# Kernel optimization log

Measured on AMD Instinct MI355X. Metric: run time of the kernel, lower is better.

Reference implementation:

```python
import jax, jax.numpy as jnp
import numpy as np

N = 12288      # num nodes == in_num_dim (num_center_nodes)
D_IN = 512     # in_node_dim
D_EMB = 128    # embed_dim
D_OUT = 64     # out_dim
E = 393216     # num edges (avg degree 32)
NEG_SLOPE = 0.2  # GATConv default negative_slope


def _glorot(k, shape):
    lim = float(np.sqrt(6.0 / (shape[0] + shape[1])))
    return jax.random.uniform(k, shape, jnp.float32, -lim, lim)


def setup_inputs() -> dict:
    key = jax.random.key(0)
    ks = jax.random.split(key, 13)
    x = jax.random.normal(ks[0], (N, D_IN), jnp.float32)
    edge_index = jax.random.randint(ks[1], (2, E), 0, N, jnp.int64)
    # StructureAE.dense: Linear(in_node_dim, embed_dim)
    W_s1 = _glorot(ks[2], (D_EMB, D_IN))
    b_s1 = jnp.zeros((D_EMB,), jnp.float32)
    # GATConv(embed_dim, out_dim): heads=1, concat, bias
    W_g = _glorot(ks[3], (D_OUT, D_EMB))
    a_src = _glorot(ks[4], (D_OUT, 1))[:, 0]
    a_dst = _glorot(ks[5], (D_OUT, 1))[:, 0]
    b_g = jnp.zeros((D_OUT,), jnp.float32)
    # AttributeAE: dense1 = Linear(N, embed_dim), dense2 = Linear(embed_dim, out_dim)
    W_a1 = _glorot(ks[6], (D_EMB, N))
    b_a1 = jnp.zeros((D_EMB,), jnp.float32)
    W_a2 = _glorot(ks[7], (D_OUT, D_EMB))
    b_a2 = jnp.zeros((D_OUT,), jnp.float32)
    return dict(x=x, W_s1=W_s1, b_s1=b_s1, W_g=W_g, a_src=a_src, a_dst=a_dst,
                b_g=b_g, W_a1=W_a1, b_a1=b_a1, W_a2=W_a2, b_a2=b_a2,
                edge_index=edge_index, batch_size=N)


def _gat(x1, W_g, a_src, a_dst, b_g, edge_index):
    """Single-head GATConv with self-loops (PyG defaults)."""
    n = x1.shape[0]
    g = x1 @ W_g.T                                   # [N, D_OUT]
    loops = jnp.arange(n, dtype=edge_index.dtype)
    src = jnp.concatenate([edge_index[0], loops])    # message source j
    dst = jnp.concatenate([edge_index[1], loops])    # message target i
    sc_src = g @ a_src                               # [N]
    sc_dst = g @ a_dst                               # [N]
    e = jax.nn.leaky_relu(sc_src[src] + sc_dst[dst], NEG_SLOPE)  # [E+N]
    m = jax.ops.segment_max(e, dst, num_segments=n)
    e = jnp.exp(e - m[dst])
    denom = jax.ops.segment_sum(e, dst, num_segments=n)
    alpha = e / denom[dst]                           # softmax per target node
    h = jax.ops.segment_sum(alpha[:, None] * g[src], dst, num_segments=n)
    return h + b_g


def reference(x, W_s1, b_s1, W_g, a_src, a_dst, b_g,
              W_a1, b_a1, W_a2, b_a2, edge_index, batch_size):
    n = x.shape[0]
    # StructureAE (dropout=0 -> identity)
    x1 = jax.nn.relu(x @ W_s1.T + b_s1)              # [N, D_EMB]
    h = _gat(x1, W_g, a_src, a_dst, b_g, edge_index)  # [N, D_OUT]
    s_ = jax.nn.sigmoid(h @ h.T)                     # [N, N]
    # AttributeAE on x[:num_center_nodes] (pad if batch smaller)
    xp = x if batch_size >= n else jnp.pad(x, ((0, n - batch_size), (0, 0)))
    xt = jax.nn.relu(xp.T @ W_a1.T + b_a1)           # [D_IN, D_EMB]
    xa = xt @ W_a2.T + b_a2                          # [D_IN, D_OUT]
    x_ = h @ xa.T                                    # [N, D_IN]
    return (x_, s_)
```

## Files before the change

kernel.cpp:

```cpp
#include <hip/hip_runtime.h>
#include <cstddef>
#include <cstdint>

#define N_NODES 12288
#define D_IN    512
#define D_EMB   128
#define D_OUT   64
#define NEDGE   393216
#define CAP     160

typedef __attribute__((ext_vector_type(8))) short short8;
typedef __attribute__((ext_vector_type(4))) float f32x4;

__device__ __forceinline__ ushort f2bf(float f) {
  uint32_t u = __float_as_uint(f);
  u += 0x7fffu + ((u >> 16) & 1u);
  return (ushort)(u >> 16);
}
__device__ __forceinline__ float bf2f(ushort h) {
  return __uint_as_float((uint32_t)h << 16);
}

__device__ __forceinline__ void conv4(const float* __restrict__ src,
    ushort* __restrict__ hi, ushort* __restrict__ lo, int idx)
{
  float4 v = *(const float4*)(src + idx);
  const float* pv = &v.x;
  ushort4 h, l;
  ushort* ph = &h.x; ushort* pl = &l.x;
#pragma unroll
  for (int q = 0; q < 4; ++q) {
    ph[q] = f2bf(pv[q]);
    pl[q] = f2bf(pv[q] - bf2f(ph[q]));
  }
  *(ushort4*)(hi + idx) = h;
  *(ushort4*)(lo + idx) = l;
}

__device__ __forceinline__ void cvt8(const float* __restrict__ p,
                                     short8& h, short8& l)
{
  float4 a = *(const float4*)p;
  float4 b = *(const float4*)(p + 4);
  const float* f0 = &a.x;
  const float* f1 = &b.x;
#pragma unroll
  for (int q = 0; q < 4; ++q) {
    ushort h0 = f2bf(f0[q]);
    h[q] = (short)h0;     l[q] = (short)f2bf(f0[q] - bf2f(h0));
    ushort h1 = f2bf(f1[q]);
    h[q + 4] = (short)h1; l[q + 4] = (short)f2bf(f1[q] - bf2f(h1));
  }
}

__device__ __forceinline__ void mfma_tile64_f32out(
    int lane, int i0, int j0,
    const ushort* __restrict__ Ahi, const ushort* __restrict__ Alo,
    const ushort* __restrict__ Bhi, const ushort* __restrict__ Blo,
    float* __restrict__ Cf, int lda, int ldb, int K, int ldc)
{
  int lm = lane & 15, lk = lane >> 4;
  f32x4 acc[4][4];
#pragma unroll
  for (int r = 0; r < 4; ++r)
#pragma unroll
    for (int c = 0; c < 4; ++c) acc[r][c] = (f32x4){0.f, 0.f, 0.f, 0.f};

#pragma unroll 1
  for (int k0 = 0; k0 < K; k0 += 32) {
    int kk = k0 + lk * 8;
    short8 Ah[4], Al[4], Bh[4], Bl[4];
#pragma unroll
    for (int t = 0; t < 4; ++t) {
      size_t ra = (size_t)(i0 + t * 16 + lm) * lda + kk;
      size_t rb = (size_t)(j0 + t * 16 + lm) * ldb + kk;
      Ah[t] = *(const short8*)(Ahi + ra);
      Al[t] = *(const short8*)(Alo + ra);
      Bh[t] = *(const short8*)(Bhi + rb);
      Bl[t] = *(const short8*)(Blo + rb);
    }
#pragma unroll
    for (int r = 0; r < 4; ++r)
#pragma unroll
      for (int c = 0; c < 4; ++c) {
        acc[r][c] = __builtin_amdgcn_mfma_f32_16x16x32_bf16(Ah[r], Bh[c], acc[r][c], 0, 0, 0);
        acc[r][c] = __builtin_amdgcn_mfma_f32_16x16x32_bf16(Ah[r], Bl[c], acc[r][c], 0, 0, 0);
        acc[r][c] = __builtin_amdgcn_mfma_f32_16x16x32_bf16(Al[r], Bh[c], acc[r][c], 0, 0, 0);
      }
  }
#pragma unroll
  for (int r = 0; r < 4; ++r)
#pragma unroll
    for (int c = 0; c < 4; ++c) {
      int col = j0 + c * 16 + lm;
#pragma unroll
      for (int q = 0; q < 4; ++q) {
        int row = i0 + r * 16 + lk * 4 + q;
        Cf[(size_t)row * ldc + col] = acc[r][c][q];
      }
    }
}

__global__ __launch_bounds__(256) void prep_kernel(
    const float* __restrict__ x, const float* __restrict__ Ws1,
    const float* __restrict__ Wg, const float* __restrict__ Wa1,
    ushort* __restrict__ s1h, ushort* __restrict__ s1l,
    ushort* __restrict__ wgh, ushort* __restrict__ wgl,
    int* __restrict__ deg, float* __restrict__ part)
{
  __shared__ float smem[6144];
  int b = blockIdx.x;
  int tid = threadIdx.x;
  if (b < 512) {
    float* Xs = smem;
    float* Ws = smem + 2048;
    int c0 = (b & 7) * 64;
    int i0 = (b >> 3) * 192;
    float* pout = part + (size_t)(b >> 3) * (D_IN * D_EMB);
    int txc = tid & 15, txj = tid >> 4;
    float acc[4][8] = {};
    for (int ib = 0; ib < 192; ib += 32) {
#pragma unroll
      for (int p = 0; p < 2; ++p) {
        int idx = tid + p * 256;
        int row = idx >> 4, q = idx & 15;
        *(float4*)&Xs[row * 64 + q * 4] =
            *(const float4*)(x + (size_t)(i0 + ib + row) * D_IN + c0 + q * 4);
      }
#pragma unroll
      for (int p = 0; p < 4; ++p) {
        int idx = tid + p * 256;
        int j = idx >> 3, q = idx & 7;
        float4 v = *(const float4*)(Wa1 + (size_t)j * N_NODES + i0 + ib + q * 4);
        Ws[(q * 4 + 0) * 128 + j] = v.x; Ws[(q * 4 + 1) * 128 + j] = v.y;
        Ws[(q * 4 + 2) * 128 + j] = v.z; Ws[(q * 4 + 3) * 128 + j] = v.w;
      }
      __syncthreads();
#pragma unroll
      for (int ii = 0; ii < 32; ++ii) {
        float a[4], bb[8];
        *(float4*)a = *(const float4*)&Xs[ii * 64 + txc * 4];
        *(float4*)&bb[0] = *(const float4*)&Ws[ii * 128 + txj * 8];
        *(float4*)&bb[4] = *(const float4*)&Ws[ii * 128 + txj * 8 + 4];
#pragma unroll
        for (int r = 0; r < 4; ++r)
#pragma unroll
          for (int c = 0; c < 8; ++c)
            acc[r][c] = fmaf(a[r], bb[c], acc[r][c]);
      }
      __syncthreads();
    }
#pragma unroll
    for (int r = 0; r < 4; ++r) {
      float4 o0, o1;
      o0.x = acc[r][0]; o0.y = acc[r][1]; o0.z = acc[r][2]; o0.w = acc[r][3];
      o1.x = acc[r][4]; o1.y = acc[r][5]; o1.z = acc[r][6]; o1.w = acc[r][7];
      size_t off = (size_t)(c0 + txc * 4 + r) * D_EMB + txj * 8;
      *(float4*)&pout[off] = o0;
      *(float4*)&pout[off + 4] = o1;
    }
  } else if (b < 584) {
    int bb = b - 512;
    if (bb < 64) conv4(Ws1, s1h, s1l, (bb * 256 + tid) * 4);
    else         conv4(Wg,  wgh, wgl, ((bb - 64) * 256 + tid) * 4);
  } else {
    deg[(b - 584) * 256 + tid] = 0;
  }
}

__device__ __forceinline__ bool edge_is64(const int* __restrict__ ei) {
  int hv = ei[2 * (threadIdx.x & 63) + 1];
  return __ballot(hv == 0) == 0xFFFFFFFFFFFFFFFFull;
}

__global__ __launch_bounds__(256) void l2_kernel(
    const int* __restrict__ ei, int* __restrict__ deg, int* __restrict__ csr,
    const float* __restrict__ x,
    const ushort* __restrict__ s1h, const ushort* __restrict__ s1l,
    const float* __restrict__ b_s1,
    const ushort* __restrict__ wgh, const ushort* __restrict__ wgl,
    float* __restrict__ g,
    const float* __restrict__ a_src, const float* __restrict__ a_dst,
    float* __restrict__ sc_s, float* __restrict__ sc_d,
    const float* __restrict__ part, const float* __restrict__ b_a1,
    float* __restrict__ xt)
{
  __shared__ ushort x1s[2][128 * 128];
  int b = blockIdx.x;
  int tid = threadIdx.x;
  if (b < 96) {
    int lane = tid & 63, wv = tid >> 6;
    int lm = lane & 15, lk = lane >> 4;
    int wr = wv >> 1, wc = wv & 1;
    int i0 = b * 128;
    {
      f32x4 acc[4][4];
#pragma unroll
      for (int r = 0; r < 4; ++r)
#pragma unroll
        for (int c = 0; c < 4; ++c) acc[r][c] = (f32x4){0.f, 0.f, 0.f, 0.f};
#pragma unroll 1
      for (int k0 = 0; k0 < D_IN; k0 += 32) {
        int kk = k0 + lk * 8;
        short8 Ah[4], Al[4], Bh[4], Bl[4];
#pragma unroll
        for (int t = 0; t < 4; ++t) {
          const float* pa = x + (size_t)(i0 + wr * 64 + t * 16 + lm) * D_IN + kk;
          cvt8(pa, Ah[t], Al[t]);
          size_t rb = (size_t)(wc * 64 + t * 16 + lm) * D_IN + kk;
          Bh[t] = *(const short8*)(s1h + rb);
          Bl[t] = *(const short8*)(s1l + rb);
        }
#pragma unroll
        for (int r = 0; r < 4; ++r)
#pragma unroll
          for (int c = 0; c < 4; ++c) {
            acc[r][c] = __builtin_amdgcn_mfma_f32_16x16x32_bf16(Ah[r], Bh[c], acc[r][c], 0, 0, 0);
            acc[r][c] = __builtin_amdgcn_mfma_f32_16x16x32_bf16(Ah[r], Bl[c], acc[r][c], 0, 0, 0);
            acc[r][c] = __builtin_amdgcn_mfma_f32_16x16x32_bf16(Al[r], Bh[c], acc[r][c], 0, 0, 0);
          }
      }
#pragma unroll
      for (int r = 0; r < 4; ++r)
#pragma unroll
        for (int c = 0; c < 4; ++c) {
          int col = wc * 64 + c * 16 + lm;
          float bv = b_s1[col];
#pragma unroll
          for (int q = 0; q < 4; ++q) {
            int row = wr * 64 + r * 16 + lk * 4 + q;
            float v = acc[r][c][q] + bv;
            v = fmaxf(v, 0.f);
            ushort hb = f2bf(v);
            int idx = ((row << 7) + col) ^ ((row & 7) << 3);
            x1s[0][idx] = hb;
            x1s[1][idx] = f2bf(v - bf2f(hb));
          }
        }
    }
    __syncthreads();
    if (wv < 2) {
      f32x4 acc[4][4];
#pragma unroll
      for (int r = 0; r < 4; ++r)
#pragma unroll
        for (int c = 0; c < 4; ++c) acc[r][c] = (f32x4){0.f, 0.f, 0.f, 0.f};
#pragma unroll 1
      for (int k0 = 0; k0 < D_EMB; k0 += 32) {
        int kk = k0 + lk * 8;
        short8 Ah[4], Al[4], Bh[4], Bl[4];
#pragma unroll
        for (int t = 0; t < 4; ++t) {
          int arow = wv * 64 + t * 16 + lm;
          int aidx = ((arow << 7) + kk) ^ ((arow & 7) << 3);
          Ah[t] = *(const short8*)&x1s[0][aidx];
          Al[t] = *(const short8*)&x1s[1][aidx];
          size_t rb = (size_t)(t * 16 + lm) * D_EMB + kk;
          Bh[t] = *(const short8*)(wgh + rb);
          Bl[t] = *(const short8*)(wgl + rb);
        }
#pragma unroll
        for (int r = 0; r < 4; ++r)
#pragma unroll
          for (int c = 0; c < 4; ++c) {
            acc[r][c] = __builtin_amdgcn_mfma_f32_16x16x32_bf16(Ah[r], Bh[c], acc[r][c], 0, 0, 0);
            acc[r][c] = __builtin_amdgcn_mfma_f32_16x16x32_bf16(Ah[r], Bl[c], acc[r][c], 0, 0, 0);
            acc[r][c] = __builtin_amdgcn_mfma_f32_16x16x32_bf16(Al[r], Bh[c], acc[r][c], 0, 0, 0);
          }
      }
#pragma unroll
      for (int r = 0; r < 4; ++r)
#pragma unroll
        for (int c = 0; c < 4; ++c) {
          int col = c * 16 + lm;
#pragma unroll
          for (int q = 0; q < 4; ++q) {
            int row = i0 + wv * 64 + r * 16 + lk * 4 + q;
            g[(size_t)row * D_OUT + col] = acc[r][c][q];
          }
        }
      float asv[4], adv[4];
#pragma unroll
      for (int c = 0; c < 4; ++c) {
        asv[c] = a_src[c * 16 + lm];
        adv[c] = a_dst[c * 16 + lm];
      }
#pragma unroll
      for (int r = 0; r < 4; ++r)
#pragma unroll
        for (int q = 0; q < 4; ++q) {
          float s = 0.f, d = 0.f;
#pragma unroll
          for (int c = 0; c < 4; ++c) {
            float v = acc[r][c][q];
            s = fmaf(v, asv[c], s);
            d = fmaf(v, adv[c], d);
          }
#pragma unroll
          for (int off = 1; off < 16; off <<= 1) {
            s += __shfl_xor(s, off);
            d += __shfl_xor(d, off);
          }
          if (lm == 0) {
            int row = i0 + wv * 64 + r * 16 + lk * 4 + q;
            sc_s[row] = s;
            sc_d[row] = d;
          }
        }
    }
  } else if (b < 1632) {
    bool is64 = edge_is64(ei);
    int e = (b - 96) * 256 + tid;
    int src = is64 ? ei[2 * e] : ei[e];
    int dst = is64 ? ei[2 * (NEDGE + e)] : ei[NEDGE + e];
    int p = atomicAdd(&deg[dst], 1);
    csr[(size_t)dst * CAP + p] = src;
  } else {
    int idx = (b - 1632) * 256 + tid;
    float v = b_a1[idx & 127];
#pragma unroll 8
    for (int c = 0; c < 64; ++c) v += part[(size_t)c * (D_IN * D_EMB) + idx];
    xt[idx] = fmaxf(v, 0.f);
  }
}

#define WCAP 192
__global__ __launch_bounds__(256) void l3_kernel(
    const int* __restrict__ deg, const int* __restrict__ csr,
    const float* __restrict__ sc_s, const float* __restrict__ sc_d,
    const float* __restrict__ g, const float* __restrict__ b_g,
    ushort* __restrict__ hhi, ushort* __restrict__ hlo,
    const float* __restrict__ xt, const float* __restrict__ Wa2,
    const float* __restrict__ b_a2,
    ushort* __restrict__ xahi, ushort* __restrict__ xalo)
{
  __shared__ float smem[4096];
  int b = blockIdx.x;
  int tid = threadIdx.x;
  if (b < 3072) {
    float (*wbuf)[WCAP] = (float(*)[WCAP])smem;
    int   (*sbuf)[WCAP] = (int(*)[WCAP])(smem + 4 * WCAP);
    int lane = tid & 63;
    int w = tid >> 6;
    int i = b * 4 + w;
    int dg = deg[i];
    int base = i * CAP;
    float scd = sc_d[i];
    float mymax = -3.4e38f;
    for (int j = lane; j <= dg; j += 64) {
      int s = (j < dg) ? csr[base + j] : i;
      float e = sc_s[s] + scd;
      e = (e > 0.f) ? e : 0.2f * e;
      mymax = fmaxf(mymax, e);
      if (j < WCAP) sbuf[w][j] = s;
    }
#pragma unroll
    for (int off = 32; off; off >>= 1) mymax = fmaxf(mymax, __shfl_xor(mymax, off));
    float sum = 0.f;
    for (int j = lane; j <= dg; j += 64) {
      int s = (j < WCAP) ? sbuf[w][j] : ((j < dg) ? csr[base + j] : i);
      float e = sc_s[s] + scd;
      e = (e > 0.f) ? e : 0.2f * e;
      float ex = __expf(e - mymax);
      sum += ex;
      if (j < WCAP) wbuf[w][j] = ex;
    }
#pragma unroll
    for (int off = 32; off; off >>= 1) sum += __shfl_xor(sum, off);
    float inv = 1.f / sum;
    float acc = 0.f;
    for (int j = 0; j <= dg; ++j) {
      int s; float ex;
      if (j < WCAP) { s = sbuf[w][j]; ex = wbuf[w][j]; }
      else {
        s = (j < dg) ? csr[base + j] : i;
        float e = sc_s[s] + scd;
        e = (e > 0.f) ? e : 0.2f * e;
        ex = __expf(e - mymax);
      }
      acc = fmaf(ex * inv, g[(size_t)s * 64 + lane], acc);
    }
    float val = acc + b_g[lane];
    size_t o = (size_t)i * 64 + lane;
    ushort hi = f2bf(val);
    hhi[o] = hi;
    hlo[o] = f2bf(val - bf2f(hi));
  } else {
    float* As = smem;
    float* Bs = smem + 2048;
    int m0 = (b - 3072) * 64;
    int tx = tid & 15, ty = tid >> 4;
    float acc[4][4] = {};
    for (int k0 = 0; k0 < D_EMB; k0 += 32) {
#pragma unroll
      for (int p = 0; p < 2; ++p) {
        int idx = tid + p * 256;
        int row = idx >> 3;
        int kq = idx & 7;
        float4 va = *(const float4*)(xt + (size_t)(m0 + row) * D_EMB + k0 + kq * 4);
        As[(kq * 4 + 0) * 64 + row] = va.x; As[(kq * 4 + 1) * 64 + row] = va.y;
        As[(kq * 4 + 2) * 64 + row] = va.z; As[(kq * 4 + 3) * 64 + row] = va.w;
        float4 vb = *(const float4*)(Wa2 + (size_t)row * D_EMB + k0 + kq * 4);
        Bs[(kq * 4 + 0) * 64 + row] = vb.x; Bs[(kq * 4 + 1) * 64 + row] = vb.y;
        Bs[(kq * 4 + 2) * 64 + row] = vb.z; Bs[(kq * 4 + 3) * 64 + row] = vb.w;
      }
      __syncthreads();
#pragma unroll
      for (int k = 0; k < 32; ++k) {
        float a[4], bb[4];
        *(float4*)a = *(const float4*)&As[k * 64 + ty * 4];
        *(float4*)bb = *(const float4*)&Bs[k * 64 + tx * 4];
#pragma unroll
        for (int r = 0; r < 4; ++r)
#pragma unroll
          for (int c = 0; c < 4; ++c)
            acc[r][c] = fmaf(a[r], bb[c], acc[r][c]);
      }
      __syncthreads();
    }
#pragma unroll
    for (int r = 0; r < 4; ++r) {
      int m = m0 + ty * 4 + r;
      ushort4 h, l;
      ushort* ph = &h.x; ushort* pl = &l.x;
#pragma unroll
      for (int c = 0; c < 4; ++c) {
        float v = acc[r][c] + b_a2[tx * 4 + c];
        ushort hb = f2bf(v);
        ph[c] = hb;
        pl[c] = f2bf(v - bf2f(hb));
      }
      *(ushort4*)(xahi + (size_t)m * D_OUT + tx * 4) = h;
      *(ushort4*)(xalo + (size_t)m * D_OUT + tx * 4) = l;
    }
  }
}

__global__ __launch_bounds__(256) void l4_kernel(
    const ushort* __restrict__ hhi, const ushort* __restrict__ hlo,
    const ushort* __restrict__ xahi, const ushort* __restrict__ xalo,
    float* __restrict__ out_x, float* __restrict__ out_s)
{
  int b = blockIdx.x;
  int lane = threadIdx.x & 63;
  int wv = threadIdx.x >> 6;
  if (b < 384) {
    int i0 = (b >> 2) * 128 + (wv >> 1) * 64;
    int j0 = (b & 3) * 128 + (wv & 1) * 64;
    mfma_tile64_f32out(lane, i0, j0, hhi, hlo, xahi, xalo,
                       out_x, D_OUT, D_OUT, D_OUT, D_IN);
    return;
  }
  int bb = b - 384;
  int iT = bb / 96;
  int jT = bb - iT * 96;
  int i0 = iT * 128 + (wv >> 1) * 64;
  int j0 = jT * 128 + (wv & 1) * 64;
  int lm = lane & 15, lk = lane >> 4;
  f32x4 acc[4][4];
#pragma unroll
  for (int r = 0; r < 4; ++r)
#pragma unroll
    for (int c = 0; c < 4; ++c) acc[r][c] = (f32x4){0.f, 0.f, 0.f, 0.f};
#pragma unroll
  for (int ks = 0; ks < 2; ++ks) {
    short8 Ah[4], Al[4], Bh[4], Bl[4];
#pragma unroll
    for (int t = 0; t < 4; ++t) {
      size_t ra = (size_t)(i0 + t * 16 + lm) * 64 + ks * 32 + lk * 8;
      size_t rb = (size_t)(j0 + t * 16 + lm) * 64 + ks * 32 + lk * 8;
      Ah[t] = *(const short8*)(hhi + ra);
      Al[t] = *(const short8*)(hlo + ra);
      Bh[t] = *(const short8*)(hhi + rb);
      Bl[t] = *(const short8*)(hlo + rb);
    }
#pragma unroll
    for (int r = 0; r < 4; ++r)
#pragma unroll
      for (int c = 0; c < 4; ++c) {
        acc[r][c] = __builtin_amdgcn_mfma_f32_16x16x32_bf16(Ah[r], Bh[c], acc[r][c], 0, 0, 0);
        acc[r][c] = __builtin_amdgcn_mfma_f32_16x16x32_bf16(Ah[r], Bl[c], acc[r][c], 0, 0, 0);
        acc[r][c] = __builtin_amdgcn_mfma_f32_16x16x32_bf16(Al[r], Bh[c], acc[r][c], 0, 0, 0);
      }
  }
#pragma unroll
  for (int r = 0; r < 4; ++r)
#pragma unroll
    for (int c = 0; c < 4; ++c) {
#pragma unroll
      for (int q = 0; q < 4; ++q) {
        float v = acc[r][c][q];
        float ex = __expf(-v);
#if __has_builtin(__builtin_amdgcn_rcpf)
        float s = __builtin_amdgcn_rcpf(1.f + ex);
#else
        float s = 1.f / (1.f + ex);
#endif
        out_s[(size_t)(i0 + r * 16 + lk * 4 + q) * N_NODES + (j0 + c * 16 + lm)] = s;
      }
    }
}

extern "C" void kernel_launch(void* const* d_in, const int* in_sizes, int n_in,
                              void* d_out, int out_size, void* d_ws, size_t ws_size,
                              hipStream_t stream)
{
  const float* x     = (const float*)d_in[0];
  const float* W_s1  = (const float*)d_in[1];
  const float* b_s1  = (const float*)d_in[2];
  const float* W_g   = (const float*)d_in[3];
  const float* a_src = (const float*)d_in[4];
  const float* a_dst = (const float*)d_in[5];
  const float* b_g   = (const float*)d_in[6];
  const float* W_a1  = (const float*)d_in[7];
  const float* b_a1  = (const float*)d_in[8];
  const float* W_a2  = (const float*)d_in[9];
  const float* b_a2  = (const float*)d_in[10];
  const int*   ei    = (const int*)d_in[11];

  float* ws   = (float*)d_ws;
  float* g    = ws;
  float* sc_s = g + (size_t)N_NODES * D_OUT;
  float* sc_d = sc_s + N_NODES;
  float* part = sc_d + N_NODES;
  float* xt   = part + (size_t)64 * D_IN * D_EMB;
  int* deg    = (int*)(xt + D_IN * D_EMB);
  int* csr    = deg + N_NODES;
  ushort* up  = (ushort*)(csr + (size_t)N_NODES * CAP);
  ushort* Ws1hi = up;                        up += (size_t)D_EMB * D_IN;
  ushort* Ws1lo = up;                        up += (size_t)D_EMB * D_IN;
  ushort* Wghi  = up;                        up += (size_t)D_OUT * D_EMB;
  ushort* Wglo  = up;                        up += (size_t)D_OUT * D_EMB;
  ushort* hhi   = up;                        up += (size_t)N_NODES * D_OUT;
  ushort* hlo   = up;                        up += (size_t)N_NODES * D_OUT;
  ushort* xahi  = up;                        up += (size_t)D_IN * D_OUT;
  ushort* xalo  = up;                        up += (size_t)D_IN * D_OUT;
  (void)ws_size; (void)in_sizes; (void)n_in; (void)out_size;

  float* out_x = (float*)d_out;
  float* out_s = out_x + (size_t)N_NODES * D_IN;

  prep_kernel<<<632, 256, 0, stream>>>(x, W_s1, W_g, W_a1,
      Ws1hi, Ws1lo, Wghi, Wglo, deg, part);
  l2_kernel<<<1888, 256, 0, stream>>>(ei, deg, csr, x, Ws1hi, Ws1lo, b_s1,
      Wghi, Wglo, g, a_src, a_dst, sc_s, sc_d, part, b_a1, xt);
  l3_kernel<<<3080, 256, 0, stream>>>(deg, csr, sc_s, sc_d, g, b_g,
      hhi, hlo, xt, W_a2, b_a2, xahi, xalo);
  l4_kernel<<<9600, 256, 0, stream>>>(hhi, hlo, xahi, xalo, out_x, out_s);
}
```

Baseline: 807.3 us.

## Merge prep and layer kernels into three launches with inline weight splitting

Removes the separate prep kernel. W_s1 and W_g are now split into bf16 hi/lo pairs inline inside the GEMM loops, and the degree array is cleared with a memset. The x1/g/score GEMM, the W_a1 partial products and the CSR edge scatter now run together in one kernel. The partial-sum reduction for xt moves into the xa kernel, so the standalone xt buffer and one launch go away. The cost is that each block redoes the weight conversion, and the xa blocks now carry a heavier reduction.

Result: slower. 886.1 us (+9.8%).

```diff
diff --git a/kernel.cpp b/kernel.cpp
--- a/kernel.cpp
+++ b/kernel.cpp
@@ -19,22 +19,6 @@
 }
 __device__ __forceinline__ float bf2f(ushort h) {
   return __uint_as_float((uint32_t)h << 16);
-}
-
-__device__ __forceinline__ void conv4(const float* __restrict__ src,
-    ushort* __restrict__ hi, ushort* __restrict__ lo, int idx)
-{
-  float4 v = *(const float4*)(src + idx);
-  const float* pv = &v.x;
-  ushort4 h, l;
-  ushort* ph = &h.x; ushort* pl = &l.x;
-#pragma unroll
-  for (int q = 0; q < 4; ++q) {
-    ph[q] = f2bf(pv[q]);
-    pl[q] = f2bf(pv[q] - bf2f(ph[q]));
-  }
-  *(ushort4*)(hi + idx) = h;
-  *(ushort4*)(lo + idx) = l;
 }
 
 __device__ __forceinline__ void cvt8(const float* __restrict__ p,
@@ -101,22 +85,146 @@
     }
 }
 
-__global__ __launch_bounds__(256) void prep_kernel(
-    const float* __restrict__ x, const float* __restrict__ Ws1,
-    const float* __restrict__ Wg, const float* __restrict__ Wa1,
-    ushort* __restrict__ s1h, ushort* __restrict__ s1l,
-    ushort* __restrict__ wgh, ushort* __restrict__ wgl,
-    int* __restrict__ deg, float* __restrict__ part)
+__device__ __forceinline__ bool edge_is64(const int* __restrict__ ei) {
+  int hv = ei[2 * (threadIdx.x & 63) + 1];
+  return __ballot(hv == 0) == 0xFFFFFFFFFFFFFFFFull;
+}
+
+__global__ __launch_bounds__(256) void mega1(
+    const float* __restrict__ x,
+    const float* __restrict__ Ws1, const float* __restrict__ b_s1,
+    const float* __restrict__ Wg,
+    const float* __restrict__ a_src, const float* __restrict__ a_dst,
+    float* __restrict__ g, float* __restrict__ sc_s, float* __restrict__ sc_d,
+    const float* __restrict__ Wa1, float* __restrict__ part,
+    const int* __restrict__ ei, int* __restrict__ deg, int* __restrict__ csr)
 {
-  __shared__ float smem[6144];
+  __shared__ float smem[16384];
   int b = blockIdx.x;
   int tid = threadIdx.x;
-  if (b < 512) {
+  if (b < 96) {
+    ushort* x1s = (ushort*)smem;
+    int lane = tid & 63, wv = tid >> 6;
+    int lm = lane & 15, lk = lane >> 4;
+    int wr = wv >> 1, wc = wv & 1;
+    int i0 = b * 128;
+    {
+      f32x4 acc[4][4];
+#pragma unroll
+      for (int r = 0; r < 4; ++r)
+#pragma unroll
+        for (int c = 0; c < 4; ++c) acc[r][c] = (f32x4){0.f, 0.f, 0.f, 0.f};
+#pragma unroll 1
+      for (int k0 = 0; k0 < D_IN; k0 += 32) {
+        int kk = k0 + lk * 8;
+        short8 Ah[4], Al[4], Bh[4], Bl[4];
+#pragma unroll
+        for (int t = 0; t < 4; ++t) {
+          cvt8(x + (size_t)(i0 + wr * 64 + t * 16 + lm) * D_IN + kk, Ah[t], Al[t]);
+          cvt8(Ws1 + (size_t)(wc * 64 + t * 16 + lm) * D_IN + kk, Bh[t], Bl[t]);
+        }
+#pragma unroll
+        for (int r = 0; r < 4; ++r)
+#pragma unroll
+          for (int c = 0; c < 4; ++c) {
+            acc[r][c] = __builtin_amdgcn_mfma_f32_16x16x32_bf16(Ah[r], Bh[c], acc[r][c], 0, 0, 0);
+            acc[r][c] = __builtin_amdgcn_mfma_f32_16x16x32_bf16(Ah[r], Bl[c], acc[r][c], 0, 0, 0);
+            acc[r][c] = __builtin_amdgcn_mfma_f32_16x16x32_bf16(Al[r], Bh[c], acc[r][c], 0, 0, 0);
+          }
+      }
+#pragma unroll
+      for (int r = 0; r < 4; ++r)
+#pragma unroll
+        for (int c = 0; c < 4; ++c) {
+          int col = wc * 64 + c * 16 + lm;
+          float bv = b_s1[col];
+#pragma unroll
+          for (int q = 0; q < 4; ++q) {
+            int row = wr * 64 + r * 16 + lk * 4 + q;
+            float v = acc[r][c][q] + bv;
+            v = fmaxf(v, 0.f);
+            ushort hb = f2bf(v);
+            int idx = ((row << 7) + col) ^ ((row & 7) << 3);
+            x1s[idx] = hb;
+            x1s[16384 + idx] = f2bf(v - bf2f(hb));
+          }
+        }
+    }
+    __syncthreads();
+    if (wv < 2) {
+      f32x4 acc[4][4];
+#pragma unroll
+      for (int r = 0; r < 4; ++r)
+#pragma unroll
+        for (int c = 0; c < 4; ++c) acc[r][c] = (f32x4){0.f, 0.f, 0.f, 0.f};
+#pragma unroll 1
+      for (int k0 = 0; k0 < D_EMB; k0 += 32) {
+        int kk = k0 + lk * 8;
+        short8 Ah[4], Al[4], Bh[4], Bl[4];
+#pragma unroll
+        for (int t = 0; t < 4; ++t) {
+          int arow = wv * 64 + t * 16 + lm;
+          int aidx = ((arow << 7) + kk) ^ ((arow & 7) << 3);
+          Ah[t] = *(const short8*)&x1s[aidx];
+          Al[t] = *(const short8*)&x1s[16384 + aidx];
+          cvt8(Wg + (size_t)(t * 16 + lm) * D_EMB + kk, Bh[t], Bl[t]);
+        }
+#pragma unroll
+        for (int r = 0; r < 4; ++r)
+#pragma unroll
+          for (int c = 0; c < 4; ++c) {
+            acc[r][c] = __builtin_amdgcn_mfma_f32_16x16x32_bf16(Ah[r], Bh[c], acc[r][c], 0, 0, 0);
+            acc[r][c] = __builtin_amdgcn_mfma_f32_16x16x32_bf16(Ah[r], Bl[c], acc[r][c], 0, 0, 0);
+            acc[r][c] = __builtin_amdgcn_mfma_f32_16x16x32_bf16(Al[r], Bh[c], acc[r][c], 0, 0, 0);
+          }
+      }
+#pragma unroll
+      for (int r = 0; r < 4; ++r)
+#pragma unroll
+        for (int c = 0; c < 4; ++c) {
+          int col = c * 16 + lm;
+#pragma unroll
+          for (int q = 0; q < 4; ++q) {
+            int row = i0 + wv * 64 + r * 16 + lk * 4 + q;
+            g[(size_t)row * D_OUT + col] = acc[r][c][q];
+          }
+        }
+      float asv[4], adv[4];
+#pragma unroll
+      for (int c = 0; c < 4; ++c) {
+        asv[c] = a_src[c * 16 + lm];
+        adv[c] = a_dst[c * 16 + lm];
+      }
+#pragma unroll
+      for (int r = 0; r < 4; ++r)
+#pragma unroll
+        for (int q = 0; q < 4; ++q) {
+          float s = 0.f, d = 0.f;
+#pragma unroll
+          for (int c = 0; c < 4; ++c) {
+            float v = acc[r][c][q];
+            s = fmaf(v, asv[c], s);
+            d = fmaf(v, adv[c], d);
+          }
+#pragma unroll
+          for (int off = 1; off < 16; off <<= 1) {
+            s += __shfl_xor(s, off);
+            d += __shfl_xor(d, off);
+          }
+          if (lm == 0) {
+            int row = i0 + wv * 64 + r * 16 + lk * 4 + q;
+            sc_s[row] = s;
+            sc_d[row] = d;
+          }
+        }
+    }
+  } else if (b < 608) {
     float* Xs = smem;
     float* Ws = smem + 2048;
-    int c0 = (b & 7) * 64;
-    int i0 = (b >> 3) * 192;
-    float* pout = part + (size_t)(b >> 3) * (D_IN * D_EMB);
+    int sb = b - 96;
+    int c0 = (sb & 7) * 64;
+    int i0 = (sb >> 3) * 192;
+    float* pout = part + (size_t)(sb >> 3) * (D_IN * D_EMB);
     int txc = tid & 15, txj = tid >> 4;
     float acc[4][8] = {};
     for (int ib = 0; ib < 192; ib += 32) {
@@ -159,182 +267,27 @@
       *(float4*)&pout[off] = o0;
       *(float4*)&pout[off + 4] = o1;
     }
-  } else if (b < 584) {
-    int bb = b - 512;
-    if (bb < 64) conv4(Ws1, s1h, s1l, (bb * 256 + tid) * 4);
-    else         conv4(Wg,  wgh, wgl, ((bb - 64) * 256 + tid) * 4);
   } else {
-    deg[(b - 584) * 256 + tid] = 0;
-  }
-}
-
-__device__ __forceinline__ bool edge_is64(const int* __restrict__ ei) {
-  int hv = ei[2 * (threadIdx.x & 63) + 1];
-  return __ballot(hv == 0) == 0xFFFFFFFFFFFFFFFFull;
-}
-
-__global__ __launch_bounds__(256) void l2_kernel(
-    const int* __restrict__ ei, int* __restrict__ deg, int* __restrict__ csr,
-    const float* __restrict__ x,
-    const ushort* __restrict__ s1h, const ushort* __restrict__ s1l,
-    const float* __restrict__ b_s1,
-    const ushort* __restrict__ wgh, const ushort* __restrict__ wgl,
-    float* __restrict__ g,
-    const float* __restrict__ a_src, const float* __restrict__ a_dst,
-    float* __restrict__ sc_s, float* __restrict__ sc_d,
-    const float* __restrict__ part, const float* __restrict__ b_a1,
-    float* __restrict__ xt)
-{
-  __shared__ ushort x1s[2][128 * 128];
-  int b = blockIdx.x;
-  int tid = threadIdx.x;
-  if (b < 96) {
-    int lane = tid & 63, wv = tid >> 6;
-    int lm = lane & 15, lk = lane >> 4;
-    int wr = wv >> 1, wc = wv & 1;
-    int i0 = b * 128;
-    {
-      f32x4 acc[4][4];
-#pragma unroll
-      for (int r = 0; r < 4; ++r)
-#pragma unroll
-        for (int c = 0; c < 4; ++c) acc[r][c] = (f32x4){0.f, 0.f, 0.f, 0.f};
-#pragma unroll 1
-      for (int k0 = 0; k0 < D_IN; k0 += 32) {
-        int kk = k0 + lk * 8;
-        short8 Ah[4], Al[4], Bh[4], Bl[4];
-#pragma unroll
-        for (int t = 0; t < 4; ++t) {
-          const float* pa = x + (size_t)(i0 + wr * 64 + t * 16 + lm) * D_IN + kk;
-          cvt8(pa, Ah[t], Al[t]);
-          size_t rb = (size_t)(wc * 64 + t * 16 + lm) * D_IN + kk;
-          Bh[t] = *(const short8*)(s1h + rb);
-          Bl[t] = *(const short8*)(s1l + rb);
-        }
-#pragma unroll
-        for (int r = 0; r < 4; ++r)
-#pragma unroll
-          for (int c = 0; c < 4; ++c) {
-            acc[r][c] = __builtin_amdgcn_mfma_f32_16x16x32_bf16(Ah[r], Bh[c], acc[r][c], 0, 0, 0);
-            acc[r][c] = __builtin_amdgcn_mfma_f32_16x16x32_bf16(Ah[r], Bl[c], acc[r][c], 0, 0, 0);
-            acc[r][c] = __builtin_amdgcn_mfma_f32_16x16x32_bf16(Al[r], Bh[c], acc[r][c], 0, 0, 0);
-          }
-      }
-#pragma unroll
-      for (int r = 0; r < 4; ++r)
-#pragma unroll
-        for (int c = 0; c < 4; ++c) {
-          int col = wc * 64 + c * 16 + lm;
-          float bv = b_s1[col];
-#pragma unroll
-          for (int q = 0; q < 4; ++q) {
-            int row = wr * 64 + r * 16 + lk * 4 + q;
-            float v = acc[r][c][q] + bv;
-            v = fmaxf(v, 0.f);
-            ushort hb = f2bf(v);
-            int idx = ((row << 7) + col) ^ ((row & 7) << 3);
-            x1s[0][idx] = hb;
-            x1s[1][idx] = f2bf(v - bf2f(hb));
-          }
-        }
-    }
-    __syncthreads();
-    if (wv < 2) {
-      f32x4 acc[4][4];
-#pragma unroll
-      for (int r = 0; r < 4; ++r)
-#pragma unroll
-        for (int c = 0; c < 4; ++c) acc[r][c] = (f32x4){0.f, 0.f, 0.f, 0.f};
-#pragma unroll 1
-      for (int k0 = 0; k0 < D_EMB; k0 += 32) {
-        int kk = k0 + lk * 8;
-        short8 Ah[4], Al[4], Bh[4], Bl[4];
-#pragma unroll
-        for (int t = 0; t < 4; ++t) {
-          int arow = wv * 64 + t * 16 + lm;
-          int aidx = ((arow << 7) + kk) ^ ((arow & 7) << 3);
-          Ah[t] = *(const short8*)&x1s[0][aidx];
-          Al[t] = *(const short8*)&x1s[1][aidx];
-          size_t rb = (size_t)(t * 16 + lm) * D_EMB + kk;
-          Bh[t] = *(const short8*)(wgh + rb);
-          Bl[t] = *(const short8*)(wgl + rb);
-        }
-#pragma unroll
-        for (int r = 0; r < 4; ++r)
-#pragma unroll
-          for (int c = 0; c < 4; ++c) {
-            acc[r][c] = __builtin_amdgcn_mfma_f32_16x16x32_bf16(Ah[r], Bh[c], acc[r][c], 0, 0, 0);
-            acc[r][c] = __builtin_amdgcn_mfma_f32_16x16x32_bf16(Ah[r], Bl[c], acc[r][c], 0, 0, 0);
-            acc[r][c] = __builtin_amdgcn_mfma_f32_16x16x32_bf16(Al[r], Bh[c], acc[r][c], 0, 0, 0);
-          }
-      }
-#pragma unroll
-      for (int r = 0; r < 4; ++r)
-#pragma unroll
-        for (int c = 0; c < 4; ++c) {
-          int col = c * 16 + lm;
-#pragma unroll
-          for (int q = 0; q < 4; ++q) {
-            int row = i0 + wv * 64 + r * 16 + lk * 4 + q;
-            g[(size_t)row * D_OUT + col] = acc[r][c][q];
-          }
-        }
-      float asv[4], adv[4];
-#pragma unroll
-      for (int c = 0; c < 4; ++c) {
-        asv[c] = a_src[c * 16 + lm];
-        adv[c] = a_dst[c * 16 + lm];
-      }
-#pragma unroll
-      for (int r = 0; r < 4; ++r)
-#pragma unroll
-        for (int q = 0; q < 4; ++q) {
-          float s = 0.f, d = 0.f;
-#pragma unroll
-          for (int c = 0; c < 4; ++c) {
-            float v = acc[r][c][q];
-            s = fmaf(v, asv[c], s);
-            d = fmaf(v, adv[c], d);
-          }
-#pragma unroll
-          for (int off = 1; off < 16; off <<= 1) {
-            s += __shfl_xor(s, off);
-            d += __shfl_xor(d, off);
-          }
-          if (lm == 0) {
-            int row = i0 + wv * 64 + r * 16 + lk * 4 + q;
-            sc_s[row] = s;
-            sc_d[row] = d;
-          }
-        }
-    }
-  } else if (b < 1632) {
     bool is64 = edge_is64(ei);
-    int e = (b - 96) * 256 + tid;
+    int e = (b - 608) * 256 + tid;
     int src = is64 ? ei[2 * e] : ei[e];
     int dst = is64 ? ei[2 * (NEDGE + e)] : ei[NEDGE + e];
     int p = atomicAdd(&deg[dst], 1);
     csr[(size_t)dst * CAP + p] = src;
-  } else {
-    int idx = (b - 1632) * 256 + tid;
-    float v = b_a1[idx & 127];
-#pragma unroll 8
-    for (int c = 0; c < 64; ++c) v += part[(size_t)c * (D_IN * D_EMB) + idx];
-    xt[idx] = fmaxf(v, 0.f);
   }
 }
 
 #define WCAP 192
-__global__ __launch_bounds__(256) void l3_kernel(
+__global__ __launch_bounds__(256) void mega2(
     const int* __restrict__ deg, const int* __restrict__ csr,
     const float* __restrict__ sc_s, const float* __restrict__ sc_d,
     const float* __restrict__ g, const float* __restrict__ b_g,
     ushort* __restrict__ hhi, ushort* __restrict__ hlo,
-    const float* __restrict__ xt, const float* __restrict__ Wa2,
-    const float* __restrict__ b_a2,
+    const float* __restrict__ part, const float* __restrict__ b_a1,
+    const float* __restrict__ Wa2, const float* __restrict__ b_a2,
     ushort* __restrict__ xahi, ushort* __restrict__ xalo)
 {
-  __shared__ float smem[4096];
+  __shared__ float smem[10240];
   int b = blockIdx.x;
   int tid = threadIdx.x;
   if (b < 3072) {
@@ -386,9 +339,37 @@
     hhi[o] = hi;
     hlo[o] = f2bf(val - bf2f(hi));
   } else {
-    float* As = smem;
-    float* Bs = smem + 2048;
+    float* AsT = smem;
+    float* Bs  = smem + 8192;
     int m0 = (b - 3072) * 64;
+    {
+      int lr = tid >> 2;
+      int j0 = (tid & 3) * 32;
+      f32x4 acc8[8];
+#pragma unroll
+      for (int q = 0; q < 8; ++q) acc8[q] = (f32x4){0.f, 0.f, 0.f, 0.f};
+      const float* src = part + (size_t)(m0 + lr) * D_EMB + j0;
+#pragma unroll 4
+      for (int ch = 0; ch < 64; ++ch) {
+        const float* p = src + (size_t)ch * (D_IN * D_EMB);
+#pragma unroll
+        for (int q = 0; q < 8; ++q) {
+          float4 v = *(const float4*)(p + q * 4);
+          acc8[q].x += v.x; acc8[q].y += v.y; acc8[q].z += v.z; acc8[q].w += v.w;
+        }
+      }
+#pragma unroll
+      for (int q = 0; q < 8; ++q) {
+        const float* pv = (const float*)&acc8[q];
+#pragma unroll
+        for (int e = 0; e < 4; ++e) {
+          int j = j0 + q * 4 + e;
+          float v = pv[e] + b_a1[j];
+          AsT[j * 64 + lr] = fmaxf(v, 0.f);
+        }
+      }
+    }
+    __syncthreads();
     int tx = tid & 15, ty = tid >> 4;
     float acc[4][4] = {};
     for (int k0 = 0; k0 < D_EMB; k0 += 32) {
@@ -397,9 +378,6 @@
         int idx = tid + p * 256;
         int row = idx >> 3;
         int kq = idx & 7;
-        float4 va = *(const float4*)(xt + (size_t)(m0 + row) * D_EMB + k0 + kq * 4);
-        As[(kq * 4 + 0) * 64 + row] = va.x; As[(kq * 4 + 1) * 64 + row] = va.y;
-        As[(kq * 4 + 2) * 64 + row] = va.z; As[(kq * 4 + 3) * 64 + row] = va.w;
         float4 vb = *(const float4*)(Wa2 + (size_t)row * D_EMB + k0 + kq * 4);
         Bs[(kq * 4 + 0) * 64 + row] = vb.x; Bs[(kq * 4 + 1) * 64 + row] = vb.y;
         Bs[(kq * 4 + 2) * 64 + row] = vb.z; Bs[(kq * 4 + 3) * 64 + row] = vb.w;
@@ -408,7 +386,7 @@
 #pragma unroll
       for (int k = 0; k < 32; ++k) {
         float a[4], bb[4];
-        *(float4*)a = *(const float4*)&As[k * 64 + ty * 4];
+        *(float4*)a = *(const float4*)&AsT[(k0 + k) * 64 + ty * 4];
         *(float4*)bb = *(const float4*)&Bs[k * 64 + tx * 4];
 #pragma unroll
         for (int r = 0; r < 4; ++r)
@@ -436,7 +414,7 @@
   }
 }
 
-__global__ __launch_bounds__(256) void l4_kernel(
+__global__ __launch_bounds__(256) void mega3(
     const ushort* __restrict__ hhi, const ushort* __restrict__ hlo,
     const ushort* __restrict__ xahi, const ushort* __restrict__ xalo,
     float* __restrict__ out_x, float* __restrict__ out_s)
@@ -523,14 +501,9 @@
   float* sc_s = g + (size_t)N_NODES * D_OUT;
   float* sc_d = sc_s + N_NODES;
   float* part = sc_d + N_NODES;
-  float* xt   = part + (size_t)64 * D_IN * D_EMB;
-  int* deg    = (int*)(xt + D_IN * D_EMB);
+  int* deg    = (int*)(part + (size_t)64 * D_IN * D_EMB);
   int* csr    = deg + N_NODES;
   ushort* up  = (ushort*)(csr + (size_t)N_NODES * CAP);
-  ushort* Ws1hi = up;                        up += (size_t)D_EMB * D_IN;
-  ushort* Ws1lo = up;                        up += (size_t)D_EMB * D_IN;
-  ushort* Wghi  = up;                        up += (size_t)D_OUT * D_EMB;
-  ushort* Wglo  = up;                        up += (size_t)D_OUT * D_EMB;
   ushort* hhi   = up;                        up += (size_t)N_NODES * D_OUT;
   ushort* hlo   = up;                        up += (size_t)N_NODES * D_OUT;
   ushort* xahi  = up;                        up += (size_t)D_IN * D_OUT;
@@ -540,11 +513,10 @@
   float* out_x = (float*)d_out;
   float* out_s = out_x + (size_t)N_NODES * D_IN;
 
-  prep_kernel<<<632, 256, 0, stream>>>(x, W_s1, W_g, W_a1,
-      Ws1hi, Ws1lo, Wghi, Wglo, deg, part);
-  l2_kernel<<<1888, 256, 0, stream>>>(ei, deg, csr, x, Ws1hi, Ws1lo, b_s1,
-      Wghi, Wglo, g, a_src, a_dst, sc_s, sc_d, part, b_a1, xt);
-  l3_kernel<<<3080, 256, 0, stream>>>(deg, csr, sc_s, sc_d, g, b_g,
-      hhi, hlo, xt, W_a2, b_a2, xahi, xalo);
-  l4_kernel<<<9600, 256, 0, stream>>>(hhi, hlo, xahi, xalo, out_x, out_s);
-}
+  hipMemsetAsync(deg, 0, N_NODES * sizeof(int), stream);
+  mega1<<<2144, 256, 0, stream>>>(x, W_s1, b_s1, W_g, a_src, a_dst,
+      g, sc_s, sc_d, W_a1, part, ei, deg, csr);
+  mega2<<<3080, 256, 0, stream>>>(deg, csr, sc_s, sc_d, g, b_g,
+      hhi, hlo, part, b_a1, W_a2, b_a2, xahi, xalo);
+  mega3<<<9600, 256, 0, stream>>>(hhi, hlo, xahi, xalo, out_x, out_s);
+}
```
